# Kernel optimization log

Hardware: AMD Instinct MI355X
Metric: run time of the kernel (lower is better)

Reference implementation:

```python
import jax, jax.numpy as jnp
import numpy as np

K = 16

def _knn_idx(pts, k):
    # pts: [B, 3, N] -> idx [B, N, k] (self-inclusive nearest neighbors)
    inner = -2.0 * jnp.einsum('bdn,bdm->bnm', pts, pts)
    xx = jnp.sum(pts * pts, axis=1)  # [B, N]
    pd = -xx[:, :, None] - inner - xx[:, None, :]  # negative squared distance
    _, idx = jax.lax.top_k(pd, k)
    return idx

def _gather(feats, idx):
    # feats: [B, N, D], idx: [B, N, k] -> [B, N, k, D]
    return jax.vmap(lambda f, i: f[i])(feats, idx)

def _conv1x1(x, w, b):
    # x: [B, Cin, N], w: [Cout, Cin], b: [Cout]
    return jnp.einsum('oi,bin->bon', w, x) + b[None, :, None]

def _linear(x, w, b):
    # x: [B, N, Din], w: [Dout, Din]
    return jnp.einsum('bnd,od->bno', x, w) + b

def _local_cov(pts, idx):
    # pts: [B, 3, N] -> [B, 12, N]
    nb = _gather(jnp.swapaxes(pts, 1, 2), idx)  # [B, N, k, 3]
    outer = nb[:, :, 0, :, None] * nb[:, :, 1, None, :]  # [B, N, 3, 3]
    B, N = pts.shape[0], pts.shape[2]
    outer = jnp.swapaxes(outer.reshape(B, N, 9), 1, 2)  # [B, 9, N]
    return jnp.concatenate([pts, outer], axis=1)

def _local_maxpool(x, idx):
    # x: [B, D, N] -> [B, N, D]
    nb = _gather(jnp.swapaxes(x, 1, 2), idx)  # [B, N, k, D]
    return jnp.max(nb, axis=2)

def setup_inputs() -> dict:
    key = jax.random.key(0)
    ks = jax.random.split(key, 20)
    def w(k, shape):
        return jax.random.normal(k, shape, dtype=jnp.float32) * 0.05
    pts = jax.random.normal(ks[0], (8, 3, 4096), dtype=jnp.float32)
    return {
        'pts': pts,
        'm1w1': w(ks[1], (64, 12)), 'm1b1': w(ks[2], (64,)),
        'm1w2': w(ks[3], (64, 64)), 'm1b2': w(ks[4], (64,)),
        'm1w3': w(ks[5], (64, 64)), 'm1b3': w(ks[6], (64,)),
        'l1w': w(ks[7], (64, 64)), 'l1b': w(ks[8], (64,)),
        'c1w': w(ks[9], (128, 64)), 'c1b': w(ks[10], (128,)),
        'l2w': w(ks[11], (128, 128)), 'l2b': w(ks[12], (128,)),
        'c2w': w(ks[13], (1024, 128)), 'c2b': w(ks[14], (1024,)),
        'm2w1': w(ks[15], (512, 1024)), 'm2b1': w(ks[16], (512,)),
        'm2w2': w(ks[17], (512, 512)), 'm2b2': w(ks[18], (512,)),
    }

def reference(pts, m1w1, m1b1, m1w2, m1b2, m1w3, m1b3, l1w, l1b,
              c1w, c1b, l2w, l2b, c2w, c2b, m2w1, m2b1, m2w2, m2b2):
    idx = _knn_idx(pts, K)  # [B, N, k]
    x = _local_cov(pts, idx)  # [B, 12, N]
    # mlp1: three 1x1 convs with ReLU
    x = jax.nn.relu(_conv1x1(x, m1w1, m1b1))
    x = jax.nn.relu(_conv1x1(x, m1w2, m1b2))
    x = jax.nn.relu(_conv1x1(x, m1w3, m1b3))  # [B, 64, N]
    # graph layer
    x = _local_maxpool(x, idx)          # [B, N, 64]
    x = _linear(x, l1w, l1b)            # [B, N, 64]
    x = jnp.swapaxes(x, 1, 2)           # [B, 64, N]
    x = jax.nn.relu(_conv1x1(x, c1w, c1b))  # [B, 128, N]
    x = _local_maxpool(x, idx)          # [B, N, 128]
    x = _linear(x, l2w, l2b)            # [B, N, 128]
    x = jnp.swapaxes(x, 1, 2)           # [B, 128, N]
    x = _conv1x1(x, c2w, c2b)           # [B, 1024, N]
    # global max pool
    x = jnp.max(x, axis=2, keepdims=True)  # [B, 1024, 1]
    # mlp2
    x = jax.nn.relu(_conv1x1(x, m2w1, m2b1))
    x = _conv1x1(x, m2w2, m2b2)  # [B, 512, 1]
    return x.reshape(-1, 512)
```

## Files before the change

kernel.cpp:

```cpp
#include <hip/hip_runtime.h>
#include <cfloat>

#define NBATCH 8
#define NPTS   4096
#define KNN    16
#define PPB    32
#define NSL    8
#define CAP    24

typedef unsigned short u16;
typedef unsigned int   u32;
typedef __attribute__((ext_vector_type(8))) short short8;
typedef __attribute__((ext_vector_type(4))) float f32x4;

__device__ __forceinline__ float relu_f(float x) { return x > 0.f ? x : 0.f; }

__device__ __forceinline__ u32 bf16_split_pack(float v)
{
    unsigned u = __float_as_uint(v);
    unsigned hb = (u + 0x7FFFu + ((u >> 16) & 1u)) >> 16;
    float hf = __uint_as_float(hb << 16);
    float l = v - hf;
    unsigned ul = __float_as_uint(l);
    unsigned lb = (ul + 0x7FFFu + ((ul >> 16) & 1u)) >> 16;
    return (hb << 16) | (lb & 0xFFFFu);
}

__device__ __forceinline__ void unpack8(uint4 a, uint4 b, short8& h, short8& l)
{
    union { unsigned u[4]; short8 s; } H, L;
    H.u[0] = __builtin_amdgcn_perm(a.y, a.x, 0x07060302);
    H.u[1] = __builtin_amdgcn_perm(a.w, a.z, 0x07060302);
    H.u[2] = __builtin_amdgcn_perm(b.y, b.x, 0x07060302);
    H.u[3] = __builtin_amdgcn_perm(b.w, b.z, 0x07060302);
    L.u[0] = __builtin_amdgcn_perm(a.y, a.x, 0x05040100);
    L.u[1] = __builtin_amdgcn_perm(a.w, a.z, 0x05040100);
    L.u[2] = __builtin_amdgcn_perm(b.y, b.x, 0x05040100);
    L.u[3] = __builtin_amdgcn_perm(b.w, b.z, 0x05040100);
    h = H.s; l = L.s;
}

__global__ __launch_bounds__(256)
void knn_kernel(const float* __restrict__ pts, int* __restrict__ idxout)
{
    __shared__ __align__(16) float4 tile[NSL * 129];
    __shared__ float  kl[PPB * NSL * 8];
    __shared__ float  thr[PPB];
    __shared__ int    cnt[PPB];

    const int b = blockIdx.y, tid = threadIdx.x;
    const int ptl = tid >> 3, r = tid & 7;
    const int n = blockIdx.x * PPB + ptl;
    const float* pb = pts + (size_t)b * 3 * NPTS;

    const float sx = pb[n], sy = pb[NPTS + n], sz = pb[2 * NPTS + n];

    float k8[8];
#pragma unroll
    for (int s = 0; s < 8; ++s) k8[s] = -FLT_MAX;

    const float4* slice = tile + r * 129;

    for (int t = 0; t < 4; ++t) {
        if (t) __syncthreads();
        for (int i = tid; i < 1024; i += 256) {
            int j = t * 1024 + i;
            float x = pb[j], y = pb[NPTS + j], z = pb[2 * NPTS + j];
            float xx = __fadd_rn(__fadd_rn(__fmul_rn(x, x), __fmul_rn(y, y)),
                                 __fmul_rn(z, z));
            tile[(i >> 7) * 129 + (i & 127)] = make_float4(x, y, z, xx);
        }
        __syncthreads();
#pragma unroll 8
        for (int ii = 0; ii < 128; ++ii) {
            float4 c = slice[ii];
            float dt = __fmaf_rn(sx, c.x, __fmaf_rn(sy, c.y, __fmul_rn(sz, c.z)));
            float pd = __fmaf_rn(2.f, dt, -c.w);
            float old0 = k8[0];
#pragma unroll
            for (int s = 7; s >= 1; --s)
                k8[s] = __builtin_amdgcn_fmed3f(k8[s - 1], k8[s], pd);
            k8[0] = fmaxf(old0, pd);
        }
    }

#pragma unroll
    for (int s = 0; s < 8; ++s) kl[(ptl * NSL + r) * 8 + s] = k8[s];
    __syncthreads();

    if (r == 0) {
        const float* L = kl + ptl * 64;
        int p0 = 0, p1 = 0, p2 = 0, p3 = 0, p4 = 0, p5 = 0, p6 = 0, p7 = 0;
        float tv = 0.f;
        for (int o = 0; o < 16; ++o) {
            float v0 = (p0 < 8) ? L[p0]      : -FLT_MAX;
            float v1 = (p1 < 8) ? L[8 + p1]  : -FLT_MAX;
            float v2 = (p2 < 8) ? L[16 + p2] : -FLT_MAX;
            float v3 = (p3 < 8) ? L[24 + p3] : -FLT_MAX;
            float v4 = (p4 < 8) ? L[32 + p4] : -FLT_MAX;
            float v5 = (p5 < 8) ? L[40 + p5] : -FLT_MAX;
            float v6 = (p6 < 8) ? L[48 + p6] : -FLT_MAX;
            float v7 = (p7 < 8) ? L[56 + p7] : -FLT_MAX;
            float m = fmaxf(fmaxf(fmaxf(v0, v1), fmaxf(v2, v3)),
                            fmaxf(fmaxf(v4, v5), fmaxf(v6, v7)));
            tv = m;
            if      (v0 == m) ++p0;
            else if (v1 == m) ++p1;
            else if (v2 == m) ++p2;
            else if (v3 == m) ++p3;
            else if (v4 == m) ++p4;
            else if (v5 == m) ++p5;
            else if (v6 == m) ++p6;
            else              ++p7;
        }
        thr[ptl] = tv;
        cnt[ptl] = 0;
    }
    __syncthreads();
    const float myThr = thr[ptl];

    float* pv = kl;
    int*   pi = (int*)(kl + PPB * CAP);

    for (int tt = 0; tt < 4; ++tt) {
        int t = 3 - tt;
        if (tt) {
            __syncthreads();
            for (int i = tid; i < 1024; i += 256) {
                int j = t * 1024 + i;
                float x = pb[j], y = pb[NPTS + j], z = pb[2 * NPTS + j];
                float xx = __fadd_rn(__fadd_rn(__fmul_rn(x, x), __fmul_rn(y, y)),
                                     __fmul_rn(z, z));
                tile[(i >> 7) * 129 + (i & 127)] = make_float4(x, y, z, xx);
            }
            __syncthreads();
        }
#pragma unroll 8
        for (int ii = 0; ii < 128; ++ii) {
            float4 c = slice[ii];
            float dt = __fmaf_rn(sx, c.x, __fmaf_rn(sy, c.y, __fmul_rn(sz, c.z)));
            float pd = __fmaf_rn(2.f, dt, -c.w);
            if (pd >= myThr) {
                int pos = atomicAdd(&cnt[ptl], 1);
                if (pos < CAP) {
                    pv[ptl * CAP + pos] = pd;
                    pi[ptl * CAP + pos] = t * 1024 + r * 128 + ii;
                }
            }
        }
    }
    __syncthreads();

    if (tid < PPB) {
        const int np = blockIdx.x * PPB + tid;
        int* out = idxout + ((size_t)b * NPTS + np) * KNN;
        int c = cnt[tid];
        if (c <= CAP) {
            float* v  = pv + tid * CAP;
            int*   ix = pi + tid * CAP;
            for (int o = 0; o < 16; ++o) {
                int best = o;
                for (int q = o + 1; q < c; ++q) {
                    float vq = v[q], vb = v[best];
                    if (vq > vb || (vq == vb && ix[q] < ix[best])) best = q;
                }
                float tv = v[o]; v[o] = v[best]; v[best] = tv;
                int   ti = ix[o]; ix[o] = ix[best]; ix[best] = ti;
                out[o] = ix[o];
            }
        } else {
            float qx = pb[np], qy = pb[NPTS + np], qz = pb[2 * NPTS + np];
            float v16[16]; int i16[16];
#pragma unroll
            for (int s = 0; s < 16; ++s) { v16[s] = -FLT_MAX; i16[s] = 0; }
            for (int j = 0; j < NPTS; ++j) {
                float x = pb[j], y = pb[NPTS + j], z = pb[2 * NPTS + j];
                float xx = __fadd_rn(__fadd_rn(__fmul_rn(x, x), __fmul_rn(y, y)),
                                     __fmul_rn(z, z));
                float dt = __fmaf_rn(qx, x, __fmaf_rn(qy, y, __fmul_rn(qz, z)));
                float pd = __fmaf_rn(2.f, dt, -xx);
                if (pd > v16[15]) {
                    int s = 15;
                    while (s > 0 && pd > v16[s - 1]) {
                        v16[s] = v16[s - 1]; i16[s] = i16[s - 1]; --s;
                    }
                    v16[s] = pd; i16[s] = j;
                }
            }
            for (int o = 0; o < 16; ++o) out[o] = i16[o];
        }
    }
}

__global__ __launch_bounds__(256)
void cov_mlp1_kernel(const float* __restrict__ pts, const int* __restrict__ idx,
                     const float* __restrict__ w1, const float* __restrict__ b1,
                     const float* __restrict__ w2, const float* __restrict__ b2,
                     const float* __restrict__ w3, const float* __restrict__ b3,
                     float* __restrict__ h3out)
{
    __shared__ __align__(16) float cov[64 * 16];
    __shared__ __align__(16) float w1s[64 * 16];
    __shared__ __align__(16) float w2s[64 * 68];
    __shared__ __align__(16) float w3s[64 * 68];
    __shared__ __align__(16) float hA[64 * 68];
    __shared__ __align__(16) float hB[64 * 68];

    const int b = blockIdx.y, tid = threadIdx.x;
    const int n0 = blockIdx.x * 64;
    const int pq = tid >> 4, cq = tid & 15;

    for (int i = tid; i < 64 * 4; i += 256) {
        int p = i >> 2, k4 = i & 3;
        float4 v = make_float4(0.f, 0.f, 0.f, 0.f);
        if (k4 < 3) v = *(const float4*)(w1 + p * 12 + k4 * 4);
        ((float4*)(w1s + p * 16))[k4] = v;
    }
    for (int i = tid; i < 64 * 16; i += 256) {
        int p = i >> 4, k4 = i & 15;
        ((float4*)(w2s + p * 68))[k4] = ((const float4*)(w2 + p * 64))[k4];
        ((float4*)(w3s + p * 68))[k4] = ((const float4*)(w3 + p * 64))[k4];
    }
    if (tid < 64) {
        const int n = n0 + tid;
        const int* ip = idx + ((size_t)b * NPTS + n) * KNN;
        int j0 = ip[0], j1 = ip[1];
        const float* pb = pts + (size_t)b * 3 * NPTS;
        float px = pb[n],  py = pb[NPTS + n],  pz = pb[2 * NPTS + n];
        float ax = pb[j0], ay = pb[NPTS + j0], az = pb[2 * NPTS + j0];
        float bx = pb[j1], by = pb[NPTS + j1], bz = pb[2 * NPTS + j1];
        float* cv = cov + tid * 16;
        cv[0] = px; cv[1] = py; cv[2] = pz;
        cv[3] = ax * bx; cv[4]  = ax * by; cv[5]  = ax * bz;
        cv[6] = ay * bx; cv[7]  = ay * by; cv[8]  = ay * bz;
        cv[9] = az * bx; cv[10] = az * by; cv[11] = az * bz;
        cv[12] = 0.f; cv[13] = 0.f; cv[14] = 0.f; cv[15] = 0.f;
    }
    __syncthreads();

    {
        float acc[4][4];
#pragma unroll
        for (int i = 0; i < 4; ++i)
#pragma unroll
            for (int j = 0; j < 4; ++j) acc[i][j] = 0.f;
        const float4* X4 = (const float4*)cov;
        const float4* W4 = (const float4*)w1s;
#pragma unroll
        for (int k4 = 0; k4 < 4; ++k4) {
            float4 xa[4], wb[4];
#pragma unroll
            for (int i = 0; i < 4; ++i) xa[i] = X4[(pq * 4 + i) * 4 + k4];
#pragma unroll
            for (int j = 0; j < 4; ++j) wb[j] = W4[(cq + 16 * j) * 4 + k4];
#pragma unroll
            for (int i = 0; i < 4; ++i)
#pragma unroll
                for (int j = 0; j < 4; ++j)
                    acc[i][j] += xa[i].x * wb[j].x + xa[i].y * wb[j].y
                               + xa[i].z * wb[j].z + xa[i].w * wb[j].w;
        }
#pragma unroll
        for (int j = 0; j < 4; ++j) {
            int c = cq + 16 * j;
            float bias = b1[c];
#pragma unroll
            for (int i = 0; i < 4; ++i)
                hA[(pq * 4 + i) * 68 + c] = relu_f(acc[i][j] + bias);
        }
    }
    __syncthreads();

    {
        float acc[4][4];
#pragma unroll
        for (int i = 0; i < 4; ++i)
#pragma unroll
            for (int j = 0; j < 4; ++j) acc[i][j] = 0.f;
        const float4* X4 = (const float4*)hA;
        const float4* W4 = (const float4*)w2s;
        for (int k4 = 0; k4 < 16; ++k4) {
            float4 xa[4], wb[4];
#pragma unroll
            for (int i = 0; i < 4; ++i) xa[i] = X4[(pq * 4 + i) * 17 + k4];
#pragma unroll
            for (int j = 0; j < 4; ++j) wb[j] = W4[(cq + 16 * j) * 17 + k4];
#pragma unroll
            for (int i = 0; i < 4; ++i)
#pragma unroll
                for (int j = 0; j < 4; ++j)
                    acc[i][j] += xa[i].x * wb[j].x + xa[i].y * wb[j].y
                               + xa[i].z * wb[j].z + xa[i].w * wb[j].w;
        }
#pragma unroll
        for (int j = 0; j < 4; ++j) {
            int c = cq + 16 * j;
            float bias = b2[c];
#pragma unroll
            for (int i = 0; i < 4; ++i)
                hB[(pq * 4 + i) * 68 + c] = relu_f(acc[i][j] + bias);
        }
    }
    __syncthreads();

    {
        float acc[4][4];
#pragma unroll
        for (int i = 0; i < 4; ++i)
#pragma unroll
            for (int j = 0; j < 4; ++j) acc[i][j] = 0.f;
        const float4* X4 = (const float4*)hB;
        const float4* W4 = (const float4*)w3s;
        for (int k4 = 0; k4 < 16; ++k4) {
            float4 xa[4], wb[4];
#pragma unroll
            for (int i = 0; i < 4; ++i) xa[i] = X4[(pq * 4 + i) * 17 + k4];
#pragma unroll
            for (int j = 0; j < 4; ++j) wb[j] = W4[(cq + 16 * j) * 17 + k4];
#pragma unroll
            for (int i = 0; i < 4; ++i)
#pragma unroll
                for (int j = 0; j < 4; ++j)
                    acc[i][j] += xa[i].x * wb[j].x + xa[i].y * wb[j].y
                               + xa[i].z * wb[j].z + xa[i].w * wb[j].w;
        }
#pragma unroll
        for (int j = 0; j < 4; ++j) {
            int c = cq + 16 * j;
            float bias = b3[c];
#pragma unroll
            for (int i = 0; i < 4; ++i)
                h3out[((size_t)b * NPTS + n0 + pq * 4 + i) * 64 + c] =
                    relu_f(acc[i][j] + bias);
        }
    }
}

template <int DV4>
__global__ __launch_bounds__(256)
void maxpool4_kernel(const float4* __restrict__ f, const int* __restrict__ idx,
                     float4* __restrict__ out)
{
    constexpr int SH = (DV4 == 16) ? 4 : 5;
    int t = blockIdx.x * 256 + threadIdx.x;
    int d4 = t & (DV4 - 1);
    int n  = (t >> SH) & (NPTS - 1);
    int b  = t >> (SH + 12);
    const int* ip = idx + ((size_t)b * NPTS + n) * KNN;
    const float4* fb = f + (size_t)b * NPTS * DV4;
    float4 v = make_float4(-FLT_MAX, -FLT_MAX, -FLT_MAX, -FLT_MAX);
#pragma unroll
    for (int k = 0; k < KNN; ++k) {
        float4 c = fb[(size_t)ip[k] * DV4 + d4];
        v.x = fmaxf(v.x, c.x); v.y = fmaxf(v.y, c.y);
        v.z = fmaxf(v.z, c.z); v.w = fmaxf(v.w, c.w);
    }
    out[t] = v;
}

__global__ __launch_bounds__(256)
void lin_conv1_mfma(const float* __restrict__ mp1, const u32* __restrict__ l1pk,
                    const float* __restrict__ l1b, const u32* __restrict__ c1pk,
                    const float* __restrict__ c1b, float* __restrict__ y1)
{
    __shared__ __align__(16) u16 lds[24576];
    u16* Wh = lds;
    u16* Wl = lds + 8192;
    u16* Xh = lds + 16384;
    u16* Xl = lds + 20480;

    const int chunk = blockIdx.x, b = blockIdx.y;
    const int tid = threadIdx.x;
    const int lane = tid & 63, wave = tid >> 6;
    const int l15 = lane & 15, l4 = lane >> 4;
    const int wm = wave >> 1, wn = wave & 1;

    for (int u = tid; u < 512; u += 256) {
        int pt = u >> 3, seg = u & 7;
        const float* src = mp1 + ((size_t)b * NPTS + chunk * 64 + pt) * 64 + seg * 8;
        float4 a = *(const float4*)src, c = *(const float4*)(src + 4);
        float v[8] = {a.x, a.y, a.z, a.w, c.x, c.y, c.z, c.w};
        union { u16 u[8]; short8 s; } H, L;
#pragma unroll
        for (int e = 0; e < 8; ++e) {
            u32 p = bf16_split_pack(v[e]);
            H.u[e] = (u16)(p >> 16); L.u[e] = (u16)p;
        }
        int lo_ = (seg * 64 + pt) * 8;
        *(short8*)&Xh[lo_] = H.s; *(short8*)&Xl[lo_] = L.s;
    }
    for (int u = tid; u < 512; u += 256) {
        int ch = u >> 3, seg = u & 7;
        const u32* src = l1pk + ch * 64 + seg * 8;
        uint4 a = *(const uint4*)src, b4 = *(const uint4*)(src + 4);
        short8 h, l;
        unpack8(a, b4, h, l);
        int lo_ = (seg * 64 + ch) * 8;
        *(short8*)&Wh[lo_] = h; *(short8*)&Wl[lo_] = l;
    }
    __syncthreads();

    f32x4 acc1[2][2];
#pragma unroll
    for (int mt = 0; mt < 2; ++mt)
#pragma unroll
        for (int nt = 0; nt < 2; ++nt)
            acc1[mt][nt] = (f32x4){0.f, 0.f, 0.f, 0.f};

    for (int kb = 0; kb < 2; ++kb) {
        const int seg = kb * 4 + l4;
        short8 Ah[2], Al[2], Bh[2], Bl[2];
#pragma unroll
        for (int mt = 0; mt < 2; ++mt) {
            int off = (seg * 64 + wm * 32 + mt * 16 + l15) * 8;
            Ah[mt] = *(const short8*)&Wh[off];
            Al[mt] = *(const short8*)&Wl[off];
        }
#pragma unroll
        for (int nt = 0; nt < 2; ++nt) {
            int off = (seg * 64 + wn * 32 + nt * 16 + l15) * 8;
            Bh[nt] = *(const short8*)&Xh[off];
            Bl[nt] = *(const short8*)&Xl[off];
        }
#pragma unroll
        for (int mt = 0; mt < 2; ++mt)
#pragma unroll
            for (int nt = 0; nt < 2; ++nt) {
                acc1[mt][nt] = __builtin_amdgcn_mfma_f32_16x16x32_bf16(
                    Ah[mt], Bh[nt], acc1[mt][nt], 0, 0, 0);
                acc1[mt][nt] = __builtin_amdgcn_mfma_f32_16x16x32_bf16(
                    Ah[mt], Bl[nt], acc1[mt][nt], 0, 0, 0);
                acc1[mt][nt] = __builtin_amdgcn_mfma_f32_16x16x32_bf16(
                    Al[mt], Bh[nt], acc1[mt][nt], 0, 0, 0);
            }
    }
    __syncthreads();

#pragma unroll
    for (int mt = 0; mt < 2; ++mt)
#pragma unroll
        for (int nt = 0; nt < 2; ++nt) {
            int pt = wn * 32 + nt * 16 + l15;
#pragma unroll
            for (int r = 0; r < 4; ++r) {
                int ch = wm * 32 + mt * 16 + 4 * l4 + r;
                u32 p = bf16_split_pack(acc1[mt][nt][r] + l1b[ch]);
                int o = ((ch >> 3) * 64 + pt) * 8 + (ch & 7);
                Xh[o] = (u16)(p >> 16); Xl[o] = (u16)p;
            }
        }
    for (int u = tid; u < 1024; u += 256) {
        int ch = u >> 3, seg = u & 7;
        const u32* src = c1pk + ch * 64 + seg * 8;
        uint4 a = *(const uint4*)src, b4 = *(const uint4*)(src + 4);
        short8 h, l;
        unpack8(a, b4, h, l);
        int lo_ = (seg * 128 + ch) * 8;
        *(short8*)&Wh[lo_] = h; *(short8*)&Wl[lo_] = l;
    }
    __syncthreads();

    f32x4 acc2[4][2];
#pragma unroll
    for (int mt = 0; mt < 4; ++mt)
#pragma unroll
        for (int nt = 0; nt < 2; ++nt)
            acc2[mt][nt] = (f32x4){0.f, 0.f, 0.f, 0.f};

    for (int kb = 0; kb < 2; ++kb) {
        const int seg = kb * 4 + l4;
        short8 Ah[4], Al[4], Bh[2], Bl[2];
#pragma unroll
        for (int mt = 0; mt < 4; ++mt) {
            int off = (seg * 128 + wm * 64 + mt * 16 + l15) * 8;
            Ah[mt] = *(const short8*)&Wh[off];
            Al[mt] = *(const short8*)&Wl[off];
        }
#pragma unroll
        for (int nt = 0; nt < 2; ++nt) {
            int off = (seg * 64 + wn * 32 + nt * 16 + l15) * 8;
            Bh[nt] = *(const short8*)&Xh[off];
            Bl[nt] = *(const short8*)&Xl[off];
        }
#pragma unroll
        for (int mt = 0; mt < 4; ++mt)
#pragma unroll
            for (int nt = 0; nt < 2; ++nt) {
                acc2[mt][nt] = __builtin_amdgcn_mfma_f32_16x16x32_bf16(
                    Ah[mt], Bh[nt], acc2[mt][nt], 0, 0, 0);
                acc2[mt][nt] = __builtin_amdgcn_mfma_f32_16x16x32_bf16(
                    Ah[mt], Bl[nt], acc2[mt][nt], 0, 0, 0);
                acc2[mt][nt] = __builtin_amdgcn_mfma_f32_16x16x32_bf16(
                    Al[mt], Bh[nt], acc2[mt][nt], 0, 0, 0);
            }
    }
    __syncthreads();

    float* yst = (float*)lds;
#pragma unroll
    for (int mt = 0; mt < 4; ++mt)
#pragma unroll
        for (int nt = 0; nt < 2; ++nt) {
            int pt = wn * 32 + nt * 16 + l15;
#pragma unroll
            for (int r = 0; r < 4; ++r) {
                int ch = wm * 64 + mt * 16 + 4 * l4 + r;
                yst[pt * 132 + ch] = relu_f(acc2[mt][nt][r] + c1b[ch]);
            }
        }
    __syncthreads();
    for (int u = tid; u < 2048; u += 256) {
        int pt = u >> 5, q = u & 31;
        *(float4*)(y1 + ((size_t)b * NPTS + chunk * 64 + pt) * 128 + q * 4) =
            *(const float4*)(yst + pt * 132 + q * 4);
    }
}

__global__ __launch_bounds__(256)
void mp2lin2_mfma(const float* __restrict__ y1, const int* __restrict__ idx,
                  const u32* __restrict__ w2pk, const float* __restrict__ bias,
                  u32* __restrict__ xpk)
{
    __shared__ __align__(16) u16 Xh[8 * 64 * 8];
    __shared__ __align__(16) u16 Xl[8 * 64 * 8];
    __shared__ __align__(16) u16 Wh[8 * 128 * 8];
    __shared__ __align__(16) u16 Wl[8 * 128 * 8];

    const int chunk = blockIdx.x, b = blockIdx.y;
    const int tid = threadIdx.x;
    const int lane = tid & 63, wave = tid >> 6;
    const int l15 = lane & 15, l4 = lane >> 4;
    const int wm = wave >> 1, wn = wave & 1;

    f32x4 acc[4][2];
#pragma unroll
    for (int mt = 0; mt < 4; ++mt)
#pragma unroll
        for (int nt = 0; nt < 2; ++nt)
            acc[mt][nt] = (f32x4){0.f, 0.f, 0.f, 0.f};

    const int f4 = tid & 15;

    for (int h = 0; h < 2; ++h) {
        __syncthreads();

        for (int u = tid; u < 1024; u += 256) {
            int row = u & 127, seg = u >> 7;
            int go = row * 128 + h * 64 + seg * 8;
            uint4 a = *(const uint4*)&w2pk[go];
            uint4 b4 = *(const uint4*)&w2pk[go + 4];
            short8 hh, ll;
            unpack8(a, b4, hh, ll);
            int lo_ = (seg * 128 + row) * 8;
            *(short8*)&Wh[lo_] = hh; *(short8*)&Wl[lo_] = ll;
        }

        for (int pass = 0; pass < 4; ++pass) {
            int ptl = pass * 16 + (tid >> 4);
            int ptg = chunk * 64 + ptl;
            const int* ip = idx + ((size_t)b * NPTS + ptg) * KNN;
            float4 mx = make_float4(-FLT_MAX, -FLT_MAX, -FLT_MAX, -FLT_MAX);
#pragma unroll
            for (int k = 0; k < KNN; ++k) {
                const float4* src = (const float4*)
                    (y1 + ((size_t)b * NPTS + ip[k]) * 128 + h * 64);
                float4 c = src[f4];
                mx.x = fmaxf(mx.x, c.x); mx.y = fmaxf(mx.y, c.y);
                mx.z = fmaxf(mx.z, c.z); mx.w = fmaxf(mx.w, c.w);
            }
            u32 p0 = bf16_split_pack(mx.x), p1 = bf16_split_pack(mx.y);
            u32 p2 = bf16_split_pack(mx.z), p3 = bf16_split_pack(mx.w);
            int seg = f4 >> 1, eb = (f4 & 1) * 4;
            int base = (seg * 64 + ptl) * 8 + eb;
            uint2 hv, lv;
            hv.x = (p0 >> 16) | (p1 & 0xFFFF0000u);
            hv.y = (p2 >> 16) | (p3 & 0xFFFF0000u);
            lv.x = (p0 & 0xFFFFu) | (p1 << 16);
            lv.y = (p2 & 0xFFFFu) | (p3 << 16);
            *(uint2*)&Xh[base] = hv;
            *(uint2*)&Xl[base] = lv;
        }
        __syncthreads();

        for (int kbl = 0; kbl < 2; ++kbl) {
            const int seg = kbl * 4 + l4;
            short8 Ah[4], Al[4], Bh[2], Bl[2];
#pragma unroll
            for (int mt = 0; mt < 4; ++mt) {
                int off = (seg * 128 + wm * 64 + mt * 16 + l15) * 8;
                Ah[mt] = *(const short8*)&Wh[off];
                Al[mt] = *(const short8*)&Wl[off];
            }
#pragma unroll
            for (int nt = 0; nt < 2; ++nt) {
                int off = (seg * 64 + wn * 32 + nt * 16 + l15) * 8;
                Bh[nt] = *(const short8*)&Xh[off];
                Bl[nt] = *(const short8*)&Xl[off];
            }
#pragma unroll
            for (int mt = 0; mt < 4; ++mt)
#pragma unroll
                for (int nt = 0; nt < 2; ++nt) {
                    acc[mt][nt] = __builtin_amdgcn_mfma_f32_16x16x32_bf16(
                        Ah[mt], Bh[nt], acc[mt][nt], 0, 0, 0);
                    acc[mt][nt] = __builtin_amdgcn_mfma_f32_16x16x32_bf16(
                        Ah[mt], Bl[nt], acc[mt][nt], 0, 0, 0);
                    acc[mt][nt] = __builtin_amdgcn_mfma_f32_16x16x32_bf16(
                        Al[mt], Bh[nt], acc[mt][nt], 0, 0, 0);
                }
        }
    }

#pragma unroll
    for (int mt = 0; mt < 4; ++mt) {
        int ch = wm * 64 + mt * 16 + 4 * l4;
        float4 bv = *(const float4*)(bias + ch);
#pragma unroll
        for (int nt = 0; nt < 2; ++nt) {
            int ptg = chunk * 64 + wn * 32 + nt * 16 + l15;
            uint4 o;
            o.x = bf16_split_pack(acc[mt][nt][0] + bv.x);
            o.y = bf16_split_pack(acc[mt][nt][1] + bv.y);
            o.z = bf16_split_pack(acc[mt][nt][2] + bv.z);
            o.w = bf16_split_pack(acc[mt][nt][3] + bv.w);
            *(uint4*)&xpk[((size_t)b * NPTS + ptg) * 128 + ch] = o;
        }
    }
}

__global__ __launch_bounds__(256)
void wsplit_kernel(const float* __restrict__ w, u32* __restrict__ wpk)
{
    int t = blockIdx.x * 256 + threadIdx.x;
    wpk[t] = bf16_split_pack(w[t]);
}

__global__ __launch_bounds__(256)
void conv2max_mfma(const u32* __restrict__ xpk, const u32* __restrict__ wpk,
                   const float* __restrict__ bias, float* __restrict__ pmax)
{
    __shared__ __align__(16) u16 lds[4 * 16384];
    u16* Wh = lds;
    u16* Wl = lds + 16384;
    u16* Xh = lds + 2 * 16384;
    u16* Xl = lds + 3 * 16384;

    const int chunk = blockIdx.x, g = blockIdx.y, b = blockIdx.z;
    const int tid = threadIdx.x;
    const int lane = tid & 63, wave = tid >> 6;
    const int l15 = lane & 15, l4 = lane >> 4;
    const int wm = wave >> 1, wn = wave & 1;

    const u32* wp_g = wpk + (size_t)g * 128 * 128;
    const u32* xp_g = xpk + ((size_t)b * NPTS + chunk * 128) * 128;

    for (int u = tid; u < 2048; u += 256) {
        int row = u & 127, seg = u >> 7;
        int go = row * 128 + seg * 8;
        int lo_ = seg * 1024 + row * 8;
        uint4 a = *(const uint4*)&wp_g[go];
        uint4 b4 = *(const uint4*)&wp_g[go + 4];
        short8 h, l;
        unpack8(a, b4, h, l);
        *(short8*)&Wh[lo_] = h; *(short8*)&Wl[lo_] = l;
        a = *(const uint4*)&xp_g[go];
        b4 = *(const uint4*)&xp_g[go + 4];
        unpack8(a, b4, h, l);
        *(short8*)&Xh[lo_] = h; *(short8*)&Xl[lo_] = l;
    }
    __syncthreads();

    f32x4 acc[4][4];
#pragma unroll
    for (int mt = 0; mt < 4; ++mt)
#pragma unroll
        for (int nt = 0; nt < 4; ++nt)
            acc[mt][nt] = (f32x4){0.f, 0.f, 0.f, 0.f};

    for (int kb = 0; kb < 4; ++kb) {
        const int seg = kb * 4 + l4;
        short8 Ah[4], Al[4], Bh[4], Bl[4];
#pragma unroll
        for (int mt = 0; mt < 4; ++mt) {
            int off = seg * 1024 + (wm * 64 + mt * 16 + l15) * 8;
            Ah[mt] = *(const short8*)&Wh[off];
            Al[mt] = *(const short8*)&Wl[off];
        }
#pragma unroll
        for (int nt = 0; nt < 4; ++nt) {
            int off = seg * 1024 + (wn * 64 + nt * 16 + l15) * 8;
            Bh[nt] = *(const short8*)&Xh[off];
            Bl[nt] = *(const short8*)&Xl[off];
        }
#pragma unroll
        for (int mt = 0; mt < 4; ++mt)
#pragma unroll
            for (int nt = 0; nt < 4; ++nt) {
                acc[mt][nt] = __builtin_amdgcn_mfma_f32_16x16x32_bf16(
                    Ah[mt], Bh[nt], acc[mt][nt], 0, 0, 0);
                acc[mt][nt] = __builtin_amdgcn_mfma_f32_16x16x32_bf16(
                    Ah[mt], Bl[nt], acc[mt][nt], 0, 0, 0);
                acc[mt][nt] = __builtin_amdgcn_mfma_f32_16x16x32_bf16(
                    Al[mt], Bh[nt], acc[mt][nt], 0, 0, 0);
            }
    }

    __syncthreads();
    float* smax = (float*)lds;
#pragma unroll
    for (int mt = 0; mt < 4; ++mt)
#pragma unroll
        for (int r = 0; r < 4; ++r) {
            float m = fmaxf(fmaxf(acc[mt][0][r], acc[mt][1][r]),
                            fmaxf(acc[mt][2][r], acc[mt][3][r]));
            int c = wm * 64 + mt * 16 + 4 * l4 + r;
            smax[c * 33 + wn * 16 + l15] = m;
        }
    __syncthreads();
    if (tid < 128) {
        const float* row = smax + tid * 33;
        float v = row[0];
#pragma unroll
        for (int j = 1; j < 32; ++j) v = fmaxf(v, row[j]);
        int c = g * 128 + tid;
        pmax[((size_t)b * 32 + chunk) * 1024 + c] = v + bias[c];
    }
}

__global__ __launch_bounds__(256)
void gmax_kernel(const float* __restrict__ pmax, float* __restrict__ gmax)
{
    int t = blockIdx.x * 256 + threadIdx.x;
    int b = t >> 10, ch = t & 1023;
    const float* pp = pmax + (size_t)b * 32 * 1024 + ch;
    float v = -FLT_MAX;
    for (int c = 0; c < 32; ++c) v = fmaxf(v, pp[c * 1024]);
    gmax[t] = v;
}

__global__ __launch_bounds__(128)
void mlp2a_kernel(const float* __restrict__ g, const float* __restrict__ w1,
                  const float* __restrict__ b1, float* __restrict__ h)
{
    __shared__ __align__(16) float sg[1024];
    const int b = blockIdx.y, tid = threadIdx.x;
    for (int i = tid; i < 1024; i += 128) sg[i] = g[b * 1024 + i];
    __syncthreads();
    const int ch = blockIdx.x * 128 + tid;
    const float4* xr = (const float4*)sg;
    const float4* wr = (const float4*)(w1 + (size_t)ch * 1024);
    float a0 = 0.f, a1 = 0.f, a2 = 0.f, a3 = 0.f;
    for (int k = 0; k < 256; ++k) {
        float4 w = wr[k], x = xr[k];
        a0 += w.x * x.x; a1 += w.y * x.y; a2 += w.z * x.z; a3 += w.w * x.w;
    }
    h[b * 512 + ch] = relu_f(b1[ch] + ((a0 + a1) + (a2 + a3)));
}

__global__ __launch_bounds__(128)
void mlp2b_kernel(const float* __restrict__ h, const float* __restrict__ w2,
                  const float* __restrict__ b2, float* __restrict__ out)
{
    __shared__ __align__(16) float sh[512];
    const int b = blockIdx.y, tid = threadIdx.x;
    for (int i = tid; i < 512; i += 128) sh[i] = h[b * 512 + i];
    __syncthreads();
    const int ch = blockIdx.x * 128 + tid;
    const float4* xr = (const float4*)sh;
    const float4* wr = (const float4*)(w2 + (size_t)ch * 512);
    float a0 = 0.f, a1 = 0.f, a2 = 0.f, a3 = 0.f;
    for (int k = 0; k < 128; ++k) {
        float4 w = wr[k], x = xr[k];
        a0 += w.x * x.x; a1 += w.y * x.y; a2 += w.z * x.z; a3 += w.w * x.w;
    }
    out[b * 512 + ch] = b2[ch] + ((a0 + a1) + (a2 + a3));
}

extern "C" void kernel_launch(void* const* d_in, const int* in_sizes, int n_in,
                              void* d_out, int out_size, void* d_ws, size_t ws_size,
                              hipStream_t stream)
{
    const float* pts  = (const float*)d_in[0];
    const float* m1w1 = (const float*)d_in[1];
    const float* m1b1 = (const float*)d_in[2];
    const float* m1w2 = (const float*)d_in[3];
    const float* m1b2 = (const float*)d_in[4];
    const float* m1w3 = (const float*)d_in[5];
    const float* m1b3 = (const float*)d_in[6];
    const float* l1w  = (const float*)d_in[7];
    const float* l1b  = (const float*)d_in[8];
    const float* c1w  = (const float*)d_in[9];
    const float* c1b  = (const float*)d_in[10];
    const float* l2w  = (const float*)d_in[11];
    const float* l2b  = (const float*)d_in[12];
    const float* c2w  = (const float*)d_in[13];
    const float* c2b  = (const float*)d_in[14];
    const float* m2w1 = (const float*)d_in[15];
    const float* m2b1 = (const float*)d_in[16];
    const float* m2w2 = (const float*)d_in[17];
    const float* m2b2 = (const float*)d_in[18];

    char* ws = (char*)d_ws;
    size_t off = 0;
    int*   idx   = (int*)(ws + off);   off += (size_t)NBATCH * NPTS * KNN * 4;
    float* h3    = (float*)(ws + off); off += (size_t)NBATCH * NPTS * 64 * 4;
    float* mp1   = (float*)(ws + off); off += (size_t)NBATCH * NPTS * 64 * 4;
    float* y1    = (float*)(ws + off); off += (size_t)NBATCH * NPTS * 128 * 4;
    u32*   xpk   = (u32*)(ws + off);   off += (size_t)NBATCH * NPTS * 128 * 4;
    float* pmaxb = (float*)(ws + off); off += (size_t)NBATCH * 64 * 1024 * 4;
    float* gmx   = (float*)(ws + off); off += (size_t)NBATCH * 1024 * 4;
    float* hbuf  = (float*)(ws + off); off += (size_t)NBATCH * 512 * 4;
    u32*   wpk   = (u32*)(ws + off);   off += (size_t)1024 * 128 * 4;
    u32*   w2pk  = (u32*)(ws + off);   off += (size_t)128 * 128 * 4;
    u32*   l1pk  = (u32*)(ws + off);   off += (size_t)64 * 64 * 4;
    u32*   c1pk  = (u32*)(ws + off);   off += (size_t)128 * 64 * 4;

    wsplit_kernel<<<dim3(512), 256, 0, stream>>>(c2w, wpk);
    wsplit_kernel<<<dim3(64), 256, 0, stream>>>(l2w, w2pk);
    wsplit_kernel<<<dim3(16), 256, 0, stream>>>(l1w, l1pk);
    wsplit_kernel<<<dim3(32), 256, 0, stream>>>(c1w, c1pk);
    knn_kernel<<<dim3(NPTS / PPB, NBATCH), 256, 0, stream>>>(pts, idx);
    cov_mlp1_kernel<<<dim3(64, NBATCH), 256, 0, stream>>>(pts, idx, m1w1, m1b1,
                                                          m1w2, m1b2, m1w3, m1b3, h3);
    maxpool4_kernel<16><<<dim3(NBATCH * NPTS * 16 / 256), 256, 0, stream>>>(
        (const float4*)h3, idx, (float4*)mp1);
    lin_conv1_mfma<<<dim3(64, NBATCH), 256, 0, stream>>>(mp1, l1pk, l1b,
                                                         c1pk, c1b, y1);
    mp2lin2_mfma<<<dim3(64, NBATCH), 256, 0, stream>>>(y1, idx, w2pk, l2b, xpk);
    conv2max_mfma<<<dim3(32, 8, NBATCH), 256, 0, stream>>>(xpk, wpk, c2b, pmaxb);
    gmax_kernel<<<dim3(32), 256, 0, stream>>>(pmaxb, gmx);
    mlp2a_kernel<<<dim3(4, NBATCH), 128, 0, stream>>>(gmx, m2w1, m2b1, hbuf);
    mlp2b_kernel<<<dim3(4, NBATCH), 128, 0, stream>>>(hbuf, m2w2, m2b2, (float*)d_out);
}
```

Before: 282.5 us.

## Compute KNN first-pass distance threshold with bf16-split MFMA

A new prep kernel packs each point's coordinates and squared norm into bf16 hi/lo split fragments. The KNN kernel's first pass, which finds the top-16 threshold, now computes the candidate distance matrix with 32x32x16 bf16 MFMA instead of scalar FMAs from a shared tile. Because the split-bf16 products are approximate, the threshold is lowered by a small epsilon and the candidate capacity is raised so that exact distances can be rechecked in the second, unchanged scalar pass. This moves the dot-product arithmetic onto matrix units. In exchange it adds a prep launch, extra candidates to sort, and a correctness risk if the approximation error exceeds the epsilon.

```diff
diff --git a/kernel.cpp b/kernel.cpp
--- a/kernel.cpp
+++ b/kernel.cpp
@@ -6,12 +6,14 @@
 #define KNN    16
 #define PPB    32
 #define NSL    8
-#define CAP    24
+#define CAP    32
+#define KEPS   5e-3f
 
 typedef unsigned short u16;
 typedef unsigned int   u32;
-typedef __attribute__((ext_vector_type(8))) short short8;
-typedef __attribute__((ext_vector_type(4))) float f32x4;
+typedef __attribute__((ext_vector_type(8)))  short short8;
+typedef __attribute__((ext_vector_type(4)))  float f32x4;
+typedef __attribute__((ext_vector_type(16))) float f32x16;
 
 __device__ __forceinline__ float relu_f(float x) { return x > 0.f ? x : 0.f; }
 
@@ -41,7 +43,36 @@
 }
 
 __global__ __launch_bounds__(256)
-void knn_kernel(const float* __restrict__ pts, int* __restrict__ idxout)
+void knn_prep_kernel(const float* __restrict__ pts, u16* __restrict__ cpk,
+                     u16* __restrict__ ppk)
+{
+    int t = blockIdx.x * 256 + threadIdx.x;
+    int b = t >> 12, j = t & 4095;
+    const float* pb = pts + (size_t)b * 3 * NPTS;
+    float x = pb[j], y = pb[NPTS + j], z = pb[2 * NPTS + j];
+    float xx = __fadd_rn(__fadd_rn(__fmul_rn(x, x), __fmul_rn(y, y)),
+                         __fmul_rn(z, z));
+    u32 px = bf16_split_pack(x),      py = bf16_split_pack(y);
+    u32 pz = bf16_split_pack(z);
+    u32 cx = bf16_split_pack(2.f * x), cy = bf16_split_pack(2.f * y);
+    u32 cz = bf16_split_pack(2.f * z), nx = bf16_split_pack(-xx);
+    u16 C[16] = { (u16)(cx >> 16), (u16)(cx >> 16), (u16)cx, (u16)cx,
+                  (u16)(cy >> 16), (u16)(cy >> 16), (u16)cy, (u16)cy,
+                  (u16)(cz >> 16), (u16)(cz >> 16), (u16)cz, (u16)cz,
+                  (u16)(nx >> 16), (u16)nx, 0, 0 };
+    u16 P[16] = { (u16)(px >> 16), (u16)px, (u16)(px >> 16), (u16)px,
+                  (u16)(py >> 16), (u16)py, (u16)(py >> 16), (u16)py,
+                  (u16)(pz >> 16), (u16)pz, (u16)(pz >> 16), (u16)pz,
+                  0x3F80, 0x3F80, 0, 0 };
+    u16* cd = cpk + (size_t)t * 16;
+    u16* pd_ = ppk + (size_t)t * 16;
+#pragma unroll
+    for (int s = 0; s < 16; ++s) { cd[s] = C[s]; pd_[s] = P[s]; }
+}
+
+__global__ __launch_bounds__(256)
+void knn_kernel(const float* __restrict__ pts, const u16* __restrict__ cpk,
+                const u16* __restrict__ ppk, int* __restrict__ idxout)
 {
     __shared__ __align__(16) float4 tile[NSL * 129];
     __shared__ float  kl[PPB * NSL * 8];
@@ -49,44 +80,44 @@
     __shared__ int    cnt[PPB];
 
     const int b = blockIdx.y, tid = threadIdx.x;
+    const int n0 = blockIdx.x * PPB;
+    const int lane = tid & 63, w = tid >> 6;
+    const int l31 = lane & 31, lh = lane >> 5;
+    const float* pb = pts + (size_t)b * 3 * NPTS;
+
+    {
+        const short8* Pp = (const short8*)(ppk + ((size_t)b * NPTS + n0) * 16);
+        short8 Bfrag = Pp[l31 * 2 + lh];
+
+        const short8* Cp = (const short8*)(cpk + (size_t)b * NPTS * 16);
+        float k8[8];
+#pragma unroll
+        for (int s = 0; s < 8; ++s) k8[s] = -FLT_MAX;
+
+        const int cbase = w * 1024;
+        f32x16 zero = {0.f, 0.f, 0.f, 0.f, 0.f, 0.f, 0.f, 0.f,
+                       0.f, 0.f, 0.f, 0.f, 0.f, 0.f, 0.f, 0.f};
+        for (int t = 0; t < 32; ++t) {
+            short8 Afrag = Cp[(cbase + t * 32 + l31) * 2 + lh];
+            f32x16 S = __builtin_amdgcn_mfma_f32_32x32x16_bf16(
+                Afrag, Bfrag, zero, 0, 0, 0);
+#pragma unroll
+            for (int v = 0; v < 16; ++v) {
+                float pd = S[v];
+                float old0 = k8[0];
+#pragma unroll
+                for (int s = 7; s >= 1; --s)
+                    k8[s] = __builtin_amdgcn_fmed3f(k8[s - 1], k8[s], pd);
+                k8[0] = fmaxf(old0, pd);
+            }
+        }
+        const int cid = w * 2 + lh;
+#pragma unroll
+        for (int s = 0; s < 8; ++s) kl[(l31 * NSL + cid) * 8 + s] = k8[s];
+    }
+    __syncthreads();
+
     const int ptl = tid >> 3, r = tid & 7;
-    const int n = blockIdx.x * PPB + ptl;
-    const float* pb = pts + (size_t)b * 3 * NPTS;
-
-    const float sx = pb[n], sy = pb[NPTS + n], sz = pb[2 * NPTS + n];
-
-    float k8[8];
-#pragma unroll
-    for (int s = 0; s < 8; ++s) k8[s] = -FLT_MAX;
-
-    const float4* slice = tile + r * 129;
-
-    for (int t = 0; t < 4; ++t) {
-        if (t) __syncthreads();
-        for (int i = tid; i < 1024; i += 256) {
-            int j = t * 1024 + i;
-            float x = pb[j], y = pb[NPTS + j], z = pb[2 * NPTS + j];
-            float xx = __fadd_rn(__fadd_rn(__fmul_rn(x, x), __fmul_rn(y, y)),
-                                 __fmul_rn(z, z));
-            tile[(i >> 7) * 129 + (i & 127)] = make_float4(x, y, z, xx);
-        }
-        __syncthreads();
-#pragma unroll 8
-        for (int ii = 0; ii < 128; ++ii) {
-            float4 c = slice[ii];
-            float dt = __fmaf_rn(sx, c.x, __fmaf_rn(sy, c.y, __fmul_rn(sz, c.z)));
-            float pd = __fmaf_rn(2.f, dt, -c.w);
-            float old0 = k8[0];
-#pragma unroll
-            for (int s = 7; s >= 1; --s)
-                k8[s] = __builtin_amdgcn_fmed3f(k8[s - 1], k8[s], pd);
-            k8[0] = fmaxf(old0, pd);
-        }
-    }
-
-#pragma unroll
-    for (int s = 0; s < 8; ++s) kl[(ptl * NSL + r) * 8 + s] = k8[s];
-    __syncthreads();
 
     if (r == 0) {
         const float* L = kl + ptl * 64;
@@ -113,28 +144,28 @@
             else if (v6 == m) ++p6;
             else              ++p7;
         }
-        thr[ptl] = tv;
+        thr[ptl] = tv - KEPS;
         cnt[ptl] = 0;
     }
     __syncthreads();
     const float myThr = thr[ptl];
+    const float sx = pb[n0 + ptl], sy = pb[NPTS + n0 + ptl],
+                sz = pb[2 * NPTS + n0 + ptl];
 
     float* pv = kl;
     int*   pi = (int*)(kl + PPB * CAP);
-
-    for (int tt = 0; tt < 4; ++tt) {
-        int t = 3 - tt;
-        if (tt) {
-            __syncthreads();
-            for (int i = tid; i < 1024; i += 256) {
-                int j = t * 1024 + i;
-                float x = pb[j], y = pb[NPTS + j], z = pb[2 * NPTS + j];
-                float xx = __fadd_rn(__fadd_rn(__fmul_rn(x, x), __fmul_rn(y, y)),
-                                     __fmul_rn(z, z));
-                tile[(i >> 7) * 129 + (i & 127)] = make_float4(x, y, z, xx);
-            }
-            __syncthreads();
-        }
+    const float4* slice = tile + r * 129;
+
+    for (int t = 0; t < 4; ++t) {
+        __syncthreads();
+        for (int i = tid; i < 1024; i += 256) {
+            int j = t * 1024 + i;
+            float x = pb[j], y = pb[NPTS + j], z = pb[2 * NPTS + j];
+            float xx = __fadd_rn(__fadd_rn(__fmul_rn(x, x), __fmul_rn(y, y)),
+                                 __fmul_rn(z, z));
+            tile[(i >> 7) * 129 + (i & 127)] = make_float4(x, y, z, xx);
+        }
+        __syncthreads();
 #pragma unroll 8
         for (int ii = 0; ii < 128; ++ii) {
             float4 c = slice[ii];
@@ -152,7 +183,7 @@
     __syncthreads();
 
     if (tid < PPB) {
-        const int np = blockIdx.x * PPB + tid;
+        const int np = n0 + tid;
         int* out = idxout + ((size_t)b * NPTS + np) * KNN;
         int c = cnt[tid];
         if (c <= CAP) {
@@ -814,12 +845,15 @@
     u32*   w2pk  = (u32*)(ws + off);   off += (size_t)128 * 128 * 4;
     u32*   l1pk  = (u32*)(ws + off);   off += (size_t)64 * 64 * 4;
     u32*   c1pk  = (u32*)(ws + off);   off += (size_t)128 * 64 * 4;
+    u16*   cpk   = (u16*)(ws + off);   off += (size_t)NBATCH * NPTS * 16 * 2;
+    u16*   ppk   = (u16*)(ws + off);   off += (size_t)NBATCH * NPTS * 16 * 2;
 
     wsplit_kernel<<<dim3(512), 256, 0, stream>>>(c2w, wpk);
     wsplit_kernel<<<dim3(64), 256, 0, stream>>>(l2w, w2pk);
     wsplit_kernel<<<dim3(16), 256, 0, stream>>>(l1w, l1pk);
     wsplit_kernel<<<dim3(32), 256, 0, stream>>>(c1w, c1pk);
-    knn_kernel<<<dim3(NPTS / PPB, NBATCH), 256, 0, stream>>>(pts, idx);
+    knn_prep_kernel<<<dim3(128), 256, 0, stream>>>(pts, cpk, ppk);
+    knn_kernel<<<dim3(NPTS / PPB, NBATCH), 256, 0, stream>>>(pts, cpk, ppk, idx);
     cov_mlp1_kernel<<<dim3(64, NBATCH), 256, 0, stream>>>(pts, idx, m1w1, m1b1,
                                                           m1w2, m1b2, m1w3, m1b3, h3);
     maxpool4_kernel<16><<<dim3(NBATCH * NPTS * 16 / 256), 256, 0, stream>>>(
```

Result: slower. 302.0 us (+6.9%).

## Split KNN candidate scan across 16 lanes per query with 4-deep partial lists

Applied to the files above, without the earlier changes.

The KNN kernel now gives each query point 16 threads instead of 8, so each thread scans half of a 128-candidate row and keeps a top-4 list instead of a top-8 list. The block size doubles to 512 threads. The threshold merge now combines 16 lists of 4 values to find the 16th-largest distance. This halves the per-thread serial insertion chain and register use in the hot loop, which should raise parallelism. The cost is a more expensive serial merge in one lane and looser thresholds, which can admit more candidates and overflow the CAP buffer more often.

```diff
diff --git a/kernel.cpp b/kernel.cpp
--- a/kernel.cpp
+++ b/kernel.cpp
@@ -5,7 +5,6 @@
 #define NPTS   4096
 #define KNN    16
 #define PPB    32
-#define NSL    8
 #define CAP    24
 
 typedef unsigned short u16;
@@ -40,30 +39,31 @@
     h = H.s; l = L.s;
 }
 
-__global__ __launch_bounds__(256)
+__global__ __launch_bounds__(512)
 void knn_kernel(const float* __restrict__ pts, int* __restrict__ idxout)
 {
-    __shared__ __align__(16) float4 tile[NSL * 129];
-    __shared__ float  kl[PPB * NSL * 8];
+    __shared__ __align__(16) float4 tile[8 * 129];
+    __shared__ float  kl[PPB * 16 * 4];
     __shared__ float  thr[PPB];
     __shared__ int    cnt[PPB];
 
     const int b = blockIdx.y, tid = threadIdx.x;
-    const int ptl = tid >> 3, r = tid & 7;
+    const int ptl = tid >> 4, r = tid & 15;
+    const int row = r >> 1, half = r & 1;
     const int n = blockIdx.x * PPB + ptl;
     const float* pb = pts + (size_t)b * 3 * NPTS;
 
     const float sx = pb[n], sy = pb[NPTS + n], sz = pb[2 * NPTS + n];
 
-    float k8[8];
-#pragma unroll
-    for (int s = 0; s < 8; ++s) k8[s] = -FLT_MAX;
-
-    const float4* slice = tile + r * 129;
+    float k4[4];
+#pragma unroll
+    for (int s = 0; s < 4; ++s) k4[s] = -FLT_MAX;
+
+    const float4* slice = tile + row * 129 + half * 64;
 
     for (int t = 0; t < 4; ++t) {
         if (t) __syncthreads();
-        for (int i = tid; i < 1024; i += 256) {
+        for (int i = tid; i < 1024; i += 512) {
             int j = t * 1024 + i;
             float x = pb[j], y = pb[NPTS + j], z = pb[2 * NPTS + j];
             float xx = __fadd_rn(__fadd_rn(__fmul_rn(x, x), __fmul_rn(y, y)),
@@ -72,46 +72,38 @@
         }
         __syncthreads();
 #pragma unroll 8
-        for (int ii = 0; ii < 128; ++ii) {
+        for (int ii = 0; ii < 64; ++ii) {
             float4 c = slice[ii];
             float dt = __fmaf_rn(sx, c.x, __fmaf_rn(sy, c.y, __fmul_rn(sz, c.z)));
             float pd = __fmaf_rn(2.f, dt, -c.w);
-            float old0 = k8[0];
-#pragma unroll
-            for (int s = 7; s >= 1; --s)
-                k8[s] = __builtin_amdgcn_fmed3f(k8[s - 1], k8[s], pd);
-            k8[0] = fmaxf(old0, pd);
-        }
-    }
-
-#pragma unroll
-    for (int s = 0; s < 8; ++s) kl[(ptl * NSL + r) * 8 + s] = k8[s];
+            float old0 = k4[0];
+#pragma unroll
+            for (int s = 3; s >= 1; --s)
+                k4[s] = __builtin_amdgcn_fmed3f(k4[s - 1], k4[s], pd);
+            k4[0] = fmaxf(old0, pd);
+        }
+    }
+
+#pragma unroll
+    for (int s = 0; s < 4; ++s) kl[(ptl * 16 + r) * 4 + s] = k4[s];
     __syncthreads();
 
     if (r == 0) {
         const float* L = kl + ptl * 64;
-        int p0 = 0, p1 = 0, p2 = 0, p3 = 0, p4 = 0, p5 = 0, p6 = 0, p7 = 0;
+        int pos[16];
+#pragma unroll
+        for (int l = 0; l < 16; ++l) pos[l] = 0;
         float tv = 0.f;
         for (int o = 0; o < 16; ++o) {
-            float v0 = (p0 < 8) ? L[p0]      : -FLT_MAX;
-            float v1 = (p1 < 8) ? L[8 + p1]  : -FLT_MAX;
-            float v2 = (p2 < 8) ? L[16 + p2] : -FLT_MAX;
-            float v3 = (p3 < 8) ? L[24 + p3] : -FLT_MAX;
-            float v4 = (p4 < 8) ? L[32 + p4] : -FLT_MAX;
-            float v5 = (p5 < 8) ? L[40 + p5] : -FLT_MAX;
-            float v6 = (p6 < 8) ? L[48 + p6] : -FLT_MAX;
-            float v7 = (p7 < 8) ? L[56 + p7] : -FLT_MAX;
-            float m = fmaxf(fmaxf(fmaxf(v0, v1), fmaxf(v2, v3)),
-                            fmaxf(fmaxf(v4, v5), fmaxf(v6, v7)));
-            tv = m;
-            if      (v0 == m) ++p0;
-            else if (v1 == m) ++p1;
-            else if (v2 == m) ++p2;
-            else if (v3 == m) ++p3;
-            else if (v4 == m) ++p4;
-            else if (v5 == m) ++p5;
-            else if (v6 == m) ++p6;
-            else              ++p7;
+            float best = -FLT_MAX; int bi = 0;
+#pragma unroll
+            for (int l = 0; l < 16; ++l) {
+                float v = (pos[l] < 4) ? L[l * 4 + pos[l]] : -FLT_MAX;
+                if (v > best) { best = v; bi = l; }
+            }
+#pragma unroll
+            for (int l = 0; l < 16; ++l) pos[l] += (l == bi);
+            tv = best;
         }
         thr[ptl] = tv;
         cnt[ptl] = 0;
@@ -126,7 +118,7 @@
         int t = 3 - tt;
         if (tt) {
             __syncthreads();
-            for (int i = tid; i < 1024; i += 256) {
+            for (int i = tid; i < 1024; i += 512) {
                 int j = t * 1024 + i;
                 float x = pb[j], y = pb[NPTS + j], z = pb[2 * NPTS + j];
                 float xx = __fadd_rn(__fadd_rn(__fmul_rn(x, x), __fmul_rn(y, y)),
@@ -136,7 +128,7 @@
             __syncthreads();
         }
 #pragma unroll 8
-        for (int ii = 0; ii < 128; ++ii) {
+        for (int ii = 0; ii < 64; ++ii) {
             float4 c = slice[ii];
             float dt = __fmaf_rn(sx, c.x, __fmaf_rn(sy, c.y, __fmul_rn(sz, c.z)));
             float pd = __fmaf_rn(2.f, dt, -c.w);
@@ -144,7 +136,7 @@
                 int pos = atomicAdd(&cnt[ptl], 1);
                 if (pos < CAP) {
                     pv[ptl * CAP + pos] = pd;
-                    pi[ptl * CAP + pos] = t * 1024 + r * 128 + ii;
+                    pi[ptl * CAP + pos] = t * 1024 + row * 128 + half * 64 + ii;
                 }
             }
         }
@@ -819,7 +811,7 @@
     wsplit_kernel<<<dim3(64), 256, 0, stream>>>(l2w, w2pk);
     wsplit_kernel<<<dim3(16), 256, 0, stream>>>(l1w, l1pk);
     wsplit_kernel<<<dim3(32), 256, 0, stream>>>(c1w, c1pk);
-    knn_kernel<<<dim3(NPTS / PPB, NBATCH), 256, 0, stream>>>(pts, idx);
+    knn_kernel<<<dim3(NPTS / PPB, NBATCH), 512, 0, stream>>>(pts, idx);
     cov_mlp1_kernel<<<dim3(64, NBATCH), 256, 0, stream>>>(pts, idx, m1w1, m1b1,
                                                           m1w2, m1b2, m1w3, m1b3, h3);
     maxpool4_kernel<16><<<dim3(NBATCH * NPTS * 16 / 256), 256, 0, stream>>>(
```

Measured after the change: 308.3 us. 1.09x slower.
